# Optimization experiments

Hardware: AMD Instinct MI355X
Metric: run time of the kernel (lower is better)

Reference implementation:

```python
import jax, jax.numpy as jnp
import numpy as np

B, N, DIM, H, DH, K = 2, 2048, 512, 8, 64, 32
SCALE = DH ** -0.5


def setup_inputs() -> dict:
    key = jax.random.key(0)
    ks = jax.random.split(key, 9)
    return {
        "x": jax.random.normal(ks[0], (B, N, DIM), jnp.float32),
        "mem_kv": jax.random.normal(ks[1], (B, H, N, K, 2, DH), jnp.float32),
        "mem_mask": jax.random.bernoulli(ks[2], 0.9, (B, H, N, K)),
        "Wq": jax.random.normal(ks[3], (DIM, H * DH), jnp.float32) * (DIM ** -0.5),
        "Wkv": jax.random.normal(ks[4], (DIM, 2 * DH), jnp.float32) * (DIM ** -0.5),
        "Wo": jax.random.normal(ks[5], (H * DH, DIM), jnp.float32) * ((H * DH) ** -0.5),
        "bo": jnp.zeros((DIM,), jnp.float32),
        "null_k": jax.random.normal(ks[6], (DH,), jnp.float32),
        "null_v": jax.random.normal(ks[7], (DH,), jnp.float32),
        "gate": jax.random.normal(ks[8], (H, 1, 1), jnp.float32),
    }


def reference(x, mem_kv, mem_mask, Wq, Wkv, Wo, bo, null_k, null_v, gate):
    b, n, _ = x.shape
    mask_value = -jnp.finfo(x.dtype).max

    # projections
    q = (x @ Wq).reshape(b, n, H, DH).transpose(0, 2, 1, 3)  # b h n d
    kv = x @ Wkv                                             # b n 2d
    k, v = kv[..., :DH], kv[..., DH:]                        # b n d (shared kv head)

    # local causal attention
    sim = jnp.einsum('bhid,bjd->bhij', q, k) * SCALE
    causal = jnp.triu(jnp.ones((n, n), bool), 1)
    sim = jnp.where(causal, mask_value, sim)
    attn = jax.nn.softmax(sim, axis=-1)
    local_values = jnp.einsum('bhij,bjd->bhid', attn, v)

    # kNN memory attention (retrieved keys/values are per-query)
    mem_k, mem_v = mem_kv[..., 0, :], mem_kv[..., 1, :]      # b h n k d
    nk = jnp.broadcast_to(null_k, (b, H, n, 1, DH))
    nv = jnp.broadcast_to(null_v, (b, H, n, 1, DH))
    mem_k = jnp.concatenate([nk, mem_k], axis=-2)
    mem_v = jnp.concatenate([nv, mem_v], axis=-2)
    mmask = jnp.concatenate([jnp.ones((b, H, n, 1), bool), mem_mask], axis=-1)

    sim_mem = jnp.einsum('bhid,bhijd->bhij', q, mem_k) * SCALE
    sim_mem = jnp.where(mmask, sim_mem, mask_value)
    attn_mem = jax.nn.softmax(sim_mem, axis=-1)
    mem_values = jnp.einsum('bhij,bhijd->bhid', attn_mem, mem_v)

    # gated combine of the two attention paths
    g = jax.nn.sigmoid(gate)                                 # h 1 1
    out = local_values * g + mem_values * (1.0 - g)          # b h n d
    out = out.transpose(0, 2, 1, 3).reshape(b, n, H * DH)
    return out @ Wo + bo
```

## Files before the change

### kernel.cpp

```cpp
#include <hip/hip_runtime.h>
#include <cstddef>
#include <cstdint>

#define SEQ_N  2048
#define NHEAD  8
#define DHEAD  64
#define NMEM   32
#define SCALE_F 0.125f
#define NEG_INF -3.0e38f
#define LDK 72

typedef short bf16x8 __attribute__((ext_vector_type(8)));
typedef float f32x4  __attribute__((ext_vector_type(4)));

__device__ __forceinline__ unsigned short f2bf(float f) {
  union { float f; uint32_t u; } v; v.f = f;
  uint32_t u = v.u;
  return (unsigned short)((u + 0x7fffu + ((u >> 16) & 1u)) >> 16);
}
__device__ __forceinline__ float bf2f(unsigned short us) {
  union { uint32_t u; float f; } v; v.u = ((uint32_t)us) << 16; return v.f;
}

__device__ __forceinline__ float wred_max(float v) {
#pragma unroll
  for (int o = 32; o > 0; o >>= 1) v = fmaxf(v, __shfl_xor(v, o));
  return v;
}
__device__ __forceinline__ float wred_sum(float v) {
#pragma unroll
  for (int o = 32; o > 0; o >>= 1) v += __shfl_xor(v, o);
  return v;
}

template <int MODE>
__global__ __launch_bounds__(256) void gemm64(
    const float* __restrict__ A, const float* __restrict__ Bw,
    float* __restrict__ Cf, unsigned short* __restrict__ Ck,
    unsigned short* __restrict__ Cv,
    const float* __restrict__ bias, int Kdim, int Ncols) {
  __shared__ float sA[64][17];
  __shared__ float sB[16][64];
  const int tid = threadIdx.x;
  const int tx = tid & 15, ty = tid >> 4;
  const int rowBase = blockIdx.x * 64, colBase = blockIdx.y * 64;
  float acc[4][4] = {};

  for (int k0 = 0; k0 < Kdim; k0 += 16) {
    {
      int r = tid >> 2, ks = (tid & 3) * 4;
      float4 a4 = *(const float4*)(A + (size_t)(rowBase + r) * Kdim + k0 + ks);
      sA[r][ks + 0] = a4.x; sA[r][ks + 1] = a4.y;
      sA[r][ks + 2] = a4.z; sA[r][ks + 3] = a4.w;
    }
#pragma unroll
    for (int it = 0; it < 4; ++it) {
      int kk = (tid >> 6) + it * 4, c = tid & 63;
      sB[kk][c] = Bw[(size_t)(k0 + kk) * Ncols + colBase + c];
    }
    __syncthreads();
#pragma unroll
    for (int kk = 0; kk < 16; ++kk) {
      float av[4];
#pragma unroll
      for (int u = 0; u < 4; ++u) av[u] = sA[ty * 4 + u][kk];
      float4 b4 = *(const float4*)&sB[kk][tx * 4];
#pragma unroll
      for (int u = 0; u < 4; ++u) {
        acc[u][0] += av[u] * b4.x; acc[u][1] += av[u] * b4.y;
        acc[u][2] += av[u] * b4.z; acc[u][3] += av[u] * b4.w;
      }
    }
    __syncthreads();
  }

#pragma unroll
  for (int ri = 0; ri < 4; ++ri) {
    int r = rowBase + ty * 4 + ri;
#pragma unroll
    for (int ci = 0; ci < 4; ++ci) {
      int c = colBase + tx * 4 + ci;
      float val = acc[ri][ci];
      if (MODE == 0) {
        int b = r >> 11, i = r & 2047, h = c >> 6, d = c & 63;
        Ck[(((size_t)(b * NHEAD + h)) * SEQ_N + i) * DHEAD + d] =
            f2bf(val * SCALE_F);
      } else if (MODE == 1) {
        if (c < DHEAD) {
          Ck[(size_t)r * DHEAD + c] = f2bf(val);
        } else {
          int b = r >> 11, i = r & 2047, d = c - DHEAD;
          Cv[((size_t)b * DHEAD + d) * SEQ_N + i] = f2bf(val);
        }
      } else {
        Cf[(size_t)r * 512 + c] = val + bias[c];
      }
    }
  }
}

__global__ __launch_bounds__(256) void mem_attn_kernel(
    const unsigned short* __restrict__ qb, const float* __restrict__ mem_kv,
    const int* __restrict__ mem_mask, const float* __restrict__ null_k,
    const float* __restrict__ null_v, float* __restrict__ mem_out) {
  const int w = threadIdx.x >> 6;
  const int lane = threadIdx.x & 63;
  const int row = blockIdx.x * 4 + w;
  const int g = lane >> 4;
  const int t = lane & 15;

  const float* mk = mem_kv + (size_t)row * (NMEM * 2 * DHEAD);

  ushort4 qu = *(const ushort4*)(qb + (size_t)row * DHEAD + t * 4);
  float4 nk4 = *(const float4*)(null_k + t * 4);
  float4 nv4 = *(const float4*)(null_v + t * 4);
  int mymask = (lane < NMEM) ? mem_mask[(size_t)row * NMEM + lane] : 1;

  float4 k4[8], v4[8];
#pragma unroll
  for (int i = 0; i < 8; ++i) {
    const float* kj = mk + (size_t)(i * 4 + g) * (2 * DHEAD);
    k4[i] = *(const float4*)(kj + t * 4);
    v4[i] = *(const float4*)(kj + DHEAD + t * 4);
  }

  const float q0 = bf2f(qu.x), q1 = bf2f(qu.y);
  const float q2 = bf2f(qu.z), q3 = bf2f(qu.w);

  float nsim = q0 * nk4.x + q1 * nk4.y + q2 * nk4.z + q3 * nk4.w;
  nsim += __shfl_xor(nsim, 1); nsim += __shfl_xor(nsim, 2);
  nsim += __shfl_xor(nsim, 4); nsim += __shfl_xor(nsim, 8);

  float s[8];
#pragma unroll
  for (int i = 0; i < 8; ++i) {
    float sv = q0 * k4[i].x + q1 * k4[i].y + q2 * k4[i].z + q3 * k4[i].w;
    sv += __shfl_xor(sv, 1); sv += __shfl_xor(sv, 2);
    sv += __shfl_xor(sv, 4); sv += __shfl_xor(sv, 8);
    int mj = __shfl(mymask, i * 4 + g);
    s[i] = (mj == 0) ? NEG_INF : sv;
  }

  float mloc = nsim;
#pragma unroll
  for (int i = 0; i < 8; ++i) mloc = fmaxf(mloc, s[i]);
  mloc = fmaxf(mloc, __shfl_xor(mloc, 16));
  mloc = fmaxf(mloc, __shfl_xor(mloc, 32));

  float p[8];
  float psum = 0.f;
#pragma unroll
  for (int i = 0; i < 8; ++i) { p[i] = __expf(s[i] - mloc); psum += p[i]; }
  psum += __shfl_xor(psum, 16);
  psum += __shfl_xor(psum, 32);
  const float pn = __expf(nsim - mloc);
  const float linv = 1.f / (pn + psum);

  float ax = 0.f, ay = 0.f, az = 0.f, aw = 0.f;
#pragma unroll
  for (int i = 0; i < 8; ++i) {
    float pj = p[i] * linv;
    ax += pj * v4[i].x; ay += pj * v4[i].y;
    az += pj * v4[i].z; aw += pj * v4[i].w;
  }
  ax += __shfl_xor(ax, 16); ay += __shfl_xor(ay, 16);
  az += __shfl_xor(az, 16); aw += __shfl_xor(aw, 16);
  ax += __shfl_xor(ax, 32); ay += __shfl_xor(ay, 32);
  az += __shfl_xor(az, 32); aw += __shfl_xor(aw, 32);

  const float pnl = pn * linv;
  ax += pnl * nv4.x; ay += pnl * nv4.y;
  az += pnl * nv4.z; aw += pnl * nv4.w;

  if (g == 0) {
    float4 o = {ax, ay, az, aw};
    *(float4*)(mem_out + (size_t)row * DHEAD + t * 4) = o;
  }
}

__global__ __launch_bounds__(256) void local_attn_mfma(
    const unsigned short* __restrict__ qb, const unsigned short* __restrict__ kb,
    const unsigned short* __restrict__ vtb, const float* __restrict__ mem_o,
    const float* __restrict__ gate, float* __restrict__ comb) {
  __shared__ unsigned short sK[64 * LDK];
  __shared__ unsigned short sV[64 * LDK];
  __shared__ unsigned short sP[4 * 16 * LDK];

  const int tid = threadIdx.x;
  const int w = tid >> 6, lane = tid & 63;
  const int m = lane & 15, quad = lane >> 4;
  const int bid = blockIdx.x;
  const int qt = 31 - (bid >> 4);
  const int bh = bid & 15;
  const int b = bh >> 3, h = bh & 7;
  const int qbase = qt * 64;

  const unsigned short* qp =
      qb + (((size_t)bh * SEQ_N + qbase + w * 16 + m) * DHEAD) + quad * 8;
  const bf16x8 aq0 = *(const bf16x8*)qp;
  const bf16x8 aq1 = *(const bf16x8*)(qp + 32);

  f32x4 acc[4] = {};
  float mrow[4], lrow[4];
#pragma unroll
  for (int r = 0; r < 4; ++r) { mrow[r] = NEG_INF; lrow[r] = 0.f; }

  unsigned short* sPw = &sP[w * 16 * LDK];

  for (int kt = 0; kt <= qt; ++kt) {
    const int kbase0 = kt * 64;
    __syncthreads();
#pragma unroll
    for (int it = 0; it < 2; ++it) {
      int idx = tid + it * 256;
      int row = idx >> 3, ch = idx & 7;
      *(uint4*)&sK[row * LDK + ch * 8] =
          *(const uint4*)(kb + ((size_t)b * SEQ_N + kbase0 + row) * DHEAD + ch * 8);
      *(uint4*)&sV[row * LDK + ch * 8] =
          *(const uint4*)(vtb + ((size_t)b * DHEAD + row) * SEQ_N + kbase0 + ch * 8);
    }
    __syncthreads();

    f32x4 s[4] = {};
#pragma unroll
    for (int nb = 0; nb < 4; ++nb) {
      bf16x8 bk0 = *(const bf16x8*)&sK[(nb * 16 + m) * LDK + quad * 8];
      bf16x8 bk1 = *(const bf16x8*)&sK[(nb * 16 + m) * LDK + 32 + quad * 8];
      s[nb] = __builtin_amdgcn_mfma_f32_16x16x32_bf16(aq0, bk0, s[nb], 0, 0, 0);
      s[nb] = __builtin_amdgcn_mfma_f32_16x16x32_bf16(aq1, bk1, s[nb], 0, 0, 0);
    }

    if (kt == qt) {
      int irow0 = w * 16 + quad * 4;
#pragma unroll
      for (int nb = 0; nb < 4; ++nb) {
        int j = nb * 16 + m;
#pragma unroll
        for (int r = 0; r < 4; ++r)
          if (j > irow0 + r) s[nb][r] = NEG_INF;
      }
    }

#pragma unroll
    for (int r = 0; r < 4; ++r) {
      float mx = fmaxf(fmaxf(s[0][r], s[1][r]), fmaxf(s[2][r], s[3][r]));
      mx = fmaxf(mx, __shfl_xor(mx, 1));
      mx = fmaxf(mx, __shfl_xor(mx, 2));
      mx = fmaxf(mx, __shfl_xor(mx, 4));
      mx = fmaxf(mx, __shfl_xor(mx, 8));
      float mnew = fmaxf(mrow[r], mx);
      float alpha = __expf(mrow[r] - mnew);
      mrow[r] = mnew;
      float rs = 0.f;
#pragma unroll
      for (int nb = 0; nb < 4; ++nb) {
        float p = __expf(s[nb][r] - mnew);
        s[nb][r] = p;
        rs += p;
      }
      rs += __shfl_xor(rs, 1); rs += __shfl_xor(rs, 2);
      rs += __shfl_xor(rs, 4); rs += __shfl_xor(rs, 8);
      lrow[r] = lrow[r] * alpha + rs;
#pragma unroll
      for (int db = 0; db < 4; ++db) acc[db][r] *= alpha;
    }

#pragma unroll
    for (int nb = 0; nb < 4; ++nb)
#pragma unroll
      for (int r = 0; r < 4; ++r)
        sPw[(quad * 4 + r) * LDK + nb * 16 + m] = f2bf(s[nb][r]);

    bf16x8 ap0 = *(const bf16x8*)&sPw[m * LDK + quad * 8];
    bf16x8 ap1 = *(const bf16x8*)&sPw[m * LDK + 32 + quad * 8];

#pragma unroll
    for (int db = 0; db < 4; ++db) {
      bf16x8 bv0 = *(const bf16x8*)&sV[(db * 16 + m) * LDK + quad * 8];
      bf16x8 bv1 = *(const bf16x8*)&sV[(db * 16 + m) * LDK + 32 + quad * 8];
      acc[db] = __builtin_amdgcn_mfma_f32_16x16x32_bf16(ap0, bv0, acc[db], 0, 0, 0);
      acc[db] = __builtin_amdgcn_mfma_f32_16x16x32_bf16(ap1, bv1, acc[db], 0, 0, 0);
    }
  }

  const float g = 1.f / (1.f + __expf(-gate[h]));
#pragma unroll
  for (int r = 0; r < 4; ++r) {
    int i = qbase + w * 16 + quad * 4 + r;
    float invl = 1.f / lrow[r];
#pragma unroll
    for (int db = 0; db < 4; ++db) {
      int d = db * 16 + m;
      float localv = acc[db][r] * invl;
      float memv = mem_o[((size_t)bh * SEQ_N + i) * DHEAD + d];
      comb[((size_t)(b * SEQ_N + i)) * 512 + h * DHEAD + d] =
          g * localv + (1.f - g) * memv;
    }
  }
}

extern "C" void kernel_launch(void* const* d_in, const int* in_sizes, int n_in,
                              void* d_out, int out_size, void* d_ws, size_t ws_size,
                              hipStream_t stream) {
  const float* x        = (const float*)d_in[0];
  const float* mem_kv   = (const float*)d_in[1];
  const int*   mem_mask = (const int*)d_in[2];
  const float* Wq       = (const float*)d_in[3];
  const float* Wkv      = (const float*)d_in[4];
  const float* Wo       = (const float*)d_in[5];
  const float* bo       = (const float*)d_in[6];
  const float* null_k   = (const float*)d_in[7];
  const float* null_v   = (const float*)d_in[8];
  const float* gate     = (const float*)d_in[9];
  float* out = (float*)d_out;

  unsigned short* qb  = (unsigned short*)d_ws;
  unsigned short* kbw = qb + 2097152;
  unsigned short* vtb = kbw + 262144;
  float* mem_o = (float*)(vtb + 262144);
  float* comb  = mem_o + 2097152;

  dim3 blk(256);
  gemm64<0><<<dim3(64, 8), blk, 0, stream>>>(x, Wq, nullptr, qb, nullptr, nullptr, 512, 512);
  gemm64<1><<<dim3(64, 2), blk, 0, stream>>>(x, Wkv, nullptr, kbw, vtb, nullptr, 512, 128);
  mem_attn_kernel<<<8192, blk, 0, stream>>>(qb, mem_kv, mem_mask, null_k, null_v, mem_o);
  local_attn_mfma<<<512, blk, 0, stream>>>(qb, kbw, vtb, mem_o, gate, comb);
  gemm64<2><<<dim3(64, 8), blk, 0, stream>>>(comb, Wo, out, nullptr, nullptr, bo, 512, 512);
}
```

Measured before the change: 888.4 us.

## Fuse memory attention into local attention kernel and merge QKV GEMMs

After: 846.5 us. 4.7% less time.

```diff
diff --git a/kernel.cpp b/kernel.cpp
--- a/kernel.cpp
+++ b/kernel.cpp
@@ -22,23 +22,77 @@
   union { uint32_t u; float f; } v; v.u = ((uint32_t)us) << 16; return v.f;
 }
 
-__device__ __forceinline__ float wred_max(float v) {
-#pragma unroll
-  for (int o = 32; o > 0; o >>= 1) v = fmaxf(v, __shfl_xor(v, o));
-  return v;
-}
-__device__ __forceinline__ float wred_sum(float v) {
-#pragma unroll
-  for (int o = 32; o > 0; o >>= 1) v += __shfl_xor(v, o);
-  return v;
-}
-
-template <int MODE>
-__global__ __launch_bounds__(256) void gemm64(
+__global__ __launch_bounds__(256) void gemm_qkv(
+    const float* __restrict__ A, const float* __restrict__ Wq,
+    const float* __restrict__ Wkv, unsigned short* __restrict__ qbo,
+    unsigned short* __restrict__ kbo, unsigned short* __restrict__ vto) {
+  __shared__ float sA[64][17];
+  __shared__ float sB[16][64];
+  const int tid = threadIdx.x;
+  const int tx = tid & 15, ty = tid >> 4;
+  const int rowBase = blockIdx.x * 64;
+  const int by = blockIdx.y;
+  const bool isQ = (by < 8);
+  const float* __restrict__ Bw = isQ ? Wq : Wkv;
+  const int Ncols = isQ ? 512 : 128;
+  const int colBase = (isQ ? by : (by - 8)) * 64;
+  float acc[4][4] = {};
+
+  for (int k0 = 0; k0 < 512; k0 += 16) {
+    {
+      int r = tid >> 2, ks = (tid & 3) * 4;
+      float4 a4 = *(const float4*)(A + (size_t)(rowBase + r) * 512 + k0 + ks);
+      sA[r][ks + 0] = a4.x; sA[r][ks + 1] = a4.y;
+      sA[r][ks + 2] = a4.z; sA[r][ks + 3] = a4.w;
+    }
+#pragma unroll
+    for (int it = 0; it < 4; ++it) {
+      int kk = (tid >> 6) + it * 4, c = tid & 63;
+      sB[kk][c] = Bw[(size_t)(k0 + kk) * Ncols + colBase + c];
+    }
+    __syncthreads();
+#pragma unroll
+    for (int kk = 0; kk < 16; ++kk) {
+      float av[4];
+#pragma unroll
+      for (int u = 0; u < 4; ++u) av[u] = sA[ty * 4 + u][kk];
+      float4 b4 = *(const float4*)&sB[kk][tx * 4];
+#pragma unroll
+      for (int u = 0; u < 4; ++u) {
+        acc[u][0] += av[u] * b4.x; acc[u][1] += av[u] * b4.y;
+        acc[u][2] += av[u] * b4.z; acc[u][3] += av[u] * b4.w;
+      }
+    }
+    __syncthreads();
+  }
+
+#pragma unroll
+  for (int ri = 0; ri < 4; ++ri) {
+    int r = rowBase + ty * 4 + ri;
+#pragma unroll
+    for (int ci = 0; ci < 4; ++ci) {
+      int c = colBase + tx * 4 + ci;
+      float val = acc[ri][ci];
+      int b = r >> 11, i = r & 2047;
+      if (isQ) {
+        int h = c >> 6, d = c & 63;
+        qbo[(((size_t)(b * NHEAD + h)) * SEQ_N + i) * DHEAD + d] =
+            f2bf(val * SCALE_F);
+      } else {
+        if (c < DHEAD) {
+          kbo[(size_t)r * DHEAD + c] = f2bf(val);
+        } else {
+          int d = c - DHEAD;
+          vto[((size_t)b * DHEAD + d) * SEQ_N + i] = f2bf(val);
+        }
+      }
+    }
+  }
+}
+
+__global__ __launch_bounds__(256) void gemm_out(
     const float* __restrict__ A, const float* __restrict__ Bw,
-    float* __restrict__ Cf, unsigned short* __restrict__ Ck,
-    unsigned short* __restrict__ Cv,
-    const float* __restrict__ bias, int Kdim, int Ncols) {
+    float* __restrict__ Cf, const float* __restrict__ bias) {
   __shared__ float sA[64][17];
   __shared__ float sB[16][64];
   const int tid = threadIdx.x;
@@ -46,17 +100,17 @@
   const int rowBase = blockIdx.x * 64, colBase = blockIdx.y * 64;
   float acc[4][4] = {};
 
-  for (int k0 = 0; k0 < Kdim; k0 += 16) {
+  for (int k0 = 0; k0 < 512; k0 += 16) {
     {
       int r = tid >> 2, ks = (tid & 3) * 4;
-      float4 a4 = *(const float4*)(A + (size_t)(rowBase + r) * Kdim + k0 + ks);
+      float4 a4 = *(const float4*)(A + (size_t)(rowBase + r) * 512 + k0 + ks);
       sA[r][ks + 0] = a4.x; sA[r][ks + 1] = a4.y;
       sA[r][ks + 2] = a4.z; sA[r][ks + 3] = a4.w;
     }
 #pragma unroll
     for (int it = 0; it < 4; ++it) {
       int kk = (tid >> 6) + it * 4, c = tid & 63;
-      sB[kk][c] = Bw[(size_t)(k0 + kk) * Ncols + colBase + c];
+      sB[kk][c] = Bw[(size_t)(k0 + kk) * 512 + colBase + c];
     }
     __syncthreads();
 #pragma unroll
@@ -80,111 +134,21 @@
 #pragma unroll
     for (int ci = 0; ci < 4; ++ci) {
       int c = colBase + tx * 4 + ci;
-      float val = acc[ri][ci];
-      if (MODE == 0) {
-        int b = r >> 11, i = r & 2047, h = c >> 6, d = c & 63;
-        Ck[(((size_t)(b * NHEAD + h)) * SEQ_N + i) * DHEAD + d] =
-            f2bf(val * SCALE_F);
-      } else if (MODE == 1) {
-        if (c < DHEAD) {
-          Ck[(size_t)r * DHEAD + c] = f2bf(val);
-        } else {
-          int b = r >> 11, i = r & 2047, d = c - DHEAD;
-          Cv[((size_t)b * DHEAD + d) * SEQ_N + i] = f2bf(val);
-        }
-      } else {
-        Cf[(size_t)r * 512 + c] = val + bias[c];
-      }
-    }
-  }
-}
-
-__global__ __launch_bounds__(256) void mem_attn_kernel(
-    const unsigned short* __restrict__ qb, const float* __restrict__ mem_kv,
+      Cf[(size_t)r * 512 + c] = acc[ri][ci] + bias[c];
+    }
+  }
+}
+
+__global__ __launch_bounds__(256) void attn_fused(
+    const unsigned short* __restrict__ qb, const unsigned short* __restrict__ kb,
+    const unsigned short* __restrict__ vtb, const float* __restrict__ mem_kv,
     const int* __restrict__ mem_mask, const float* __restrict__ null_k,
-    const float* __restrict__ null_v, float* __restrict__ mem_out) {
-  const int w = threadIdx.x >> 6;
-  const int lane = threadIdx.x & 63;
-  const int row = blockIdx.x * 4 + w;
-  const int g = lane >> 4;
-  const int t = lane & 15;
-
-  const float* mk = mem_kv + (size_t)row * (NMEM * 2 * DHEAD);
-
-  ushort4 qu = *(const ushort4*)(qb + (size_t)row * DHEAD + t * 4);
-  float4 nk4 = *(const float4*)(null_k + t * 4);
-  float4 nv4 = *(const float4*)(null_v + t * 4);
-  int mymask = (lane < NMEM) ? mem_mask[(size_t)row * NMEM + lane] : 1;
-
-  float4 k4[8], v4[8];
-#pragma unroll
-  for (int i = 0; i < 8; ++i) {
-    const float* kj = mk + (size_t)(i * 4 + g) * (2 * DHEAD);
-    k4[i] = *(const float4*)(kj + t * 4);
-    v4[i] = *(const float4*)(kj + DHEAD + t * 4);
-  }
-
-  const float q0 = bf2f(qu.x), q1 = bf2f(qu.y);
-  const float q2 = bf2f(qu.z), q3 = bf2f(qu.w);
-
-  float nsim = q0 * nk4.x + q1 * nk4.y + q2 * nk4.z + q3 * nk4.w;
-  nsim += __shfl_xor(nsim, 1); nsim += __shfl_xor(nsim, 2);
-  nsim += __shfl_xor(nsim, 4); nsim += __shfl_xor(nsim, 8);
-
-  float s[8];
-#pragma unroll
-  for (int i = 0; i < 8; ++i) {
-    float sv = q0 * k4[i].x + q1 * k4[i].y + q2 * k4[i].z + q3 * k4[i].w;
-    sv += __shfl_xor(sv, 1); sv += __shfl_xor(sv, 2);
-    sv += __shfl_xor(sv, 4); sv += __shfl_xor(sv, 8);
-    int mj = __shfl(mymask, i * 4 + g);
-    s[i] = (mj == 0) ? NEG_INF : sv;
-  }
-
-  float mloc = nsim;
-#pragma unroll
-  for (int i = 0; i < 8; ++i) mloc = fmaxf(mloc, s[i]);
-  mloc = fmaxf(mloc, __shfl_xor(mloc, 16));
-  mloc = fmaxf(mloc, __shfl_xor(mloc, 32));
-
-  float p[8];
-  float psum = 0.f;
-#pragma unroll
-  for (int i = 0; i < 8; ++i) { p[i] = __expf(s[i] - mloc); psum += p[i]; }
-  psum += __shfl_xor(psum, 16);
-  psum += __shfl_xor(psum, 32);
-  const float pn = __expf(nsim - mloc);
-  const float linv = 1.f / (pn + psum);
-
-  float ax = 0.f, ay = 0.f, az = 0.f, aw = 0.f;
-#pragma unroll
-  for (int i = 0; i < 8; ++i) {
-    float pj = p[i] * linv;
-    ax += pj * v4[i].x; ay += pj * v4[i].y;
-    az += pj * v4[i].z; aw += pj * v4[i].w;
-  }
-  ax += __shfl_xor(ax, 16); ay += __shfl_xor(ay, 16);
-  az += __shfl_xor(az, 16); aw += __shfl_xor(aw, 16);
-  ax += __shfl_xor(ax, 32); ay += __shfl_xor(ay, 32);
-  az += __shfl_xor(az, 32); aw += __shfl_xor(aw, 32);
-
-  const float pnl = pn * linv;
-  ax += pnl * nv4.x; ay += pnl * nv4.y;
-  az += pnl * nv4.z; aw += pnl * nv4.w;
-
-  if (g == 0) {
-    float4 o = {ax, ay, az, aw};
-    *(float4*)(mem_out + (size_t)row * DHEAD + t * 4) = o;
-  }
-}
-
-__global__ __launch_bounds__(256) void local_attn_mfma(
-    const unsigned short* __restrict__ qb, const unsigned short* __restrict__ kb,
-    const unsigned short* __restrict__ vtb, const float* __restrict__ mem_o,
-    const float* __restrict__ gate, float* __restrict__ comb) {
+    const float* __restrict__ null_v, const float* __restrict__ gate,
+    float* __restrict__ comb) {
   __shared__ unsigned short sK[64 * LDK];
   __shared__ unsigned short sV[64 * LDK];
   __shared__ unsigned short sP[4 * 16 * LDK];
+  __shared__ float sM[64][64];
 
   const int tid = threadIdx.x;
   const int w = tid >> 6, lane = tid & 63;
@@ -194,6 +158,81 @@
   const int bh = bid & 15;
   const int b = bh >> 3, h = bh & 7;
   const int qbase = qt * 64;
+
+  {
+    const int g = lane >> 4;
+    const int t = lane & 15;
+    const float4 nk4 = *(const float4*)(null_k + t * 4);
+    const float4 nv4 = *(const float4*)(null_v + t * 4);
+
+    for (int rr = 0; rr < 16; ++rr) {
+      const size_t rowg = (size_t)bh * SEQ_N + qbase + w * 16 + rr;
+      const float* mk = mem_kv + rowg * (NMEM * 2 * DHEAD);
+
+      ushort4 qu = *(const ushort4*)(qb + rowg * DHEAD + t * 4);
+      int mymask = (lane < NMEM) ? mem_mask[rowg * NMEM + lane] : 1;
+      float4 k4[8], v4[8];
+#pragma unroll
+      for (int i = 0; i < 8; ++i) {
+        const float* kj = mk + (size_t)(i * 4 + g) * (2 * DHEAD);
+        k4[i] = *(const float4*)(kj + t * 4);
+        v4[i] = *(const float4*)(kj + DHEAD + t * 4);
+      }
+
+      const float q0 = bf2f(qu.x), q1 = bf2f(qu.y);
+      const float q2 = bf2f(qu.z), q3 = bf2f(qu.w);
+
+      float nsim = q0 * nk4.x + q1 * nk4.y + q2 * nk4.z + q3 * nk4.w;
+      nsim += __shfl_xor(nsim, 1); nsim += __shfl_xor(nsim, 2);
+      nsim += __shfl_xor(nsim, 4); nsim += __shfl_xor(nsim, 8);
+
+      float s[8];
+#pragma unroll
+      for (int i = 0; i < 8; ++i) {
+        float sv = q0 * k4[i].x + q1 * k4[i].y + q2 * k4[i].z + q3 * k4[i].w;
+        sv += __shfl_xor(sv, 1); sv += __shfl_xor(sv, 2);
+        sv += __shfl_xor(sv, 4); sv += __shfl_xor(sv, 8);
+        int mj = __shfl(mymask, i * 4 + g);
+        s[i] = (mj == 0) ? NEG_INF : sv;
+      }
+
+      float mloc = nsim;
+#pragma unroll
+      for (int i = 0; i < 8; ++i) mloc = fmaxf(mloc, s[i]);
+      mloc = fmaxf(mloc, __shfl_xor(mloc, 16));
+      mloc = fmaxf(mloc, __shfl_xor(mloc, 32));
+
+      float p[8];
+      float psum = 0.f;
+#pragma unroll
+      for (int i = 0; i < 8; ++i) { p[i] = __expf(s[i] - mloc); psum += p[i]; }
+      psum += __shfl_xor(psum, 16);
+      psum += __shfl_xor(psum, 32);
+      const float pn = __expf(nsim - mloc);
+      const float linv = 1.f / (pn + psum);
+
+      float ax = 0.f, ay = 0.f, az = 0.f, aw = 0.f;
+#pragma unroll
+      for (int i = 0; i < 8; ++i) {
+        float pj = p[i] * linv;
+        ax += pj * v4[i].x; ay += pj * v4[i].y;
+        az += pj * v4[i].z; aw += pj * v4[i].w;
+      }
+      ax += __shfl_xor(ax, 16); ay += __shfl_xor(ay, 16);
+      az += __shfl_xor(az, 16); aw += __shfl_xor(aw, 16);
+      ax += __shfl_xor(ax, 32); ay += __shfl_xor(ay, 32);
+      az += __shfl_xor(az, 32); aw += __shfl_xor(aw, 32);
+
+      const float pnl = pn * linv;
+      ax += pnl * nv4.x; ay += pnl * nv4.y;
+      az += pnl * nv4.z; aw += pnl * nv4.w;
+
+      if (g == 0) {
+        float4 o = {ax, ay, az, aw};
+        *(float4*)&sM[w * 16 + rr][t * 4] = o;
+      }
+    }
+  }
 
   const unsigned short* qp =
       qb + (((size_t)bh * SEQ_N + qbase + w * 16 + m) * DHEAD) + quad * 8;
@@ -283,7 +322,7 @@
     }
   }
 
-  const float g = 1.f / (1.f + __expf(-gate[h]));
+  const float gh = 1.f / (1.f + __expf(-gate[h]));
 #pragma unroll
   for (int r = 0; r < 4; ++r) {
     int i = qbase + w * 16 + quad * 4 + r;
@@ -292,9 +331,9 @@
     for (int db = 0; db < 4; ++db) {
       int d = db * 16 + m;
       float localv = acc[db][r] * invl;
-      float memv = mem_o[((size_t)bh * SEQ_N + i) * DHEAD + d];
+      float memv = sM[w * 16 + quad * 4 + r][d];
       comb[((size_t)(b * SEQ_N + i)) * 512 + h * DHEAD + d] =
-          g * localv + (1.f - g) * memv;
+          gh * localv + (1.f - gh) * memv;
     }
   }
 }
@@ -317,13 +356,11 @@
   unsigned short* qb  = (unsigned short*)d_ws;
   unsigned short* kbw = qb + 2097152;
   unsigned short* vtb = kbw + 262144;
-  float* mem_o = (float*)(vtb + 262144);
-  float* comb  = mem_o + 2097152;
+  float* comb  = (float*)(vtb + 262144);
 
   dim3 blk(256);
-  gemm64<0><<<dim3(64, 8), blk, 0, stream>>>(x, Wq, nullptr, qb, nullptr, nullptr, 512, 512);
-  gemm64<1><<<dim3(64, 2), blk, 0, stream>>>(x, Wkv, nullptr, kbw, vtb, nullptr, 512, 128);
-  mem_attn_kernel<<<8192, blk, 0, stream>>>(qb, mem_kv, mem_mask, null_k, null_v, mem_o);
-  local_attn_mfma<<<512, blk, 0, stream>>>(qb, kbw, vtb, mem_o, gate, comb);
-  gemm64<2><<<dim3(64, 8), blk, 0, stream>>>(comb, Wo, out, nullptr, nullptr, bo, 512, 512);
-}
+  gemm_qkv<<<dim3(64, 10), blk, 0, stream>>>(x, Wq, Wkv, qb, kbw, vtb);
+  attn_fused<<<512, blk, 0, stream>>>(qb, kbw, vtb, mem_kv, mem_mask,
+                                      null_k, null_v, gate, comb);
+  gemm_out<<<dim3(64, 8), blk, 0, stream>>>(comb, Wo, out, bo);
+}
```
